# Kernel tuning notes

Hardware: AMD Instinct MI355X
Metric: run time of the kernel (lower is better)

The kernel has to match this reference:

```python
import jax, jax.numpy as jnp
import numpy as np

HEAD_NUM = 16


def setup_inputs() -> dict:
    key = jax.random.key(0)
    k1, k2, k3, k4 = jax.random.split(key, 4)
    B, S, E = 8, 1024, 1024
    inputs = jax.random.normal(k1, (B, S, E), dtype=jnp.float32)
    W_Query = jax.random.normal(k2, (E, E), dtype=jnp.float32) * 0.05
    W_Key = jax.random.normal(k3, (E, E), dtype=jnp.float32) * 0.05
    W_Value = jax.random.normal(k4, (E, E), dtype=jnp.float32) * 0.05
    return {"inputs": inputs, "W_Query": W_Query, "W_Key": W_Key, "W_Value": W_Value}


def reference(inputs, W_Query, W_Key, W_Value):
    B, S, E = inputs.shape
    H = HEAD_NUM
    D = E // H
    # QKV projections: [B,S,E] @ [E,E] -> [B,S,E]
    q = jnp.einsum('bse,ef->bsf', inputs, W_Query).reshape(B, S, H, D)
    k = jnp.einsum('bse,ef->bsf', inputs, W_Key).reshape(B, S, H, D)
    v = jnp.einsum('bse,ef->bsf', inputs, W_Value).reshape(B, S, H, D)
    # NOTE: original has NO 1/sqrt(D) scaling.
    scores = jnp.einsum('bihd,bjhd->bhij', q, k)  # [B,H,S,S]
    att = jax.nn.softmax(scores, axis=-1)
    out = jnp.einsum('bhij,bjhd->bihd', att, v).reshape(B, S, E)
    return jax.nn.relu(out)
```

## Files before the change

kernel.cpp:

```cpp
#include <hip/hip_runtime.h>
#include <cstdint>
#include <cstddef>

#define B_ 8
#define S_ 1024
#define E_ 1024
#define H_ 16
#define D_ 64
#define M_ (B_*S_)

typedef _Float16 f16;
typedef __attribute__((ext_vector_type(8))) _Float16 f16x8;
typedef __attribute__((ext_vector_type(4))) _Float16 f16x4;
typedef __attribute__((ext_vector_type(4))) float  f32x4;
typedef __attribute__((ext_vector_type(16))) float f32x16;
typedef __attribute__((ext_vector_type(4))) int    int4v;
typedef __attribute__((ext_vector_type(2))) int    int2v;

__device__ __forceinline__ f32x4 mfma16(f16x8 a, f16x8 b, f32x4 c) {
  return __builtin_amdgcn_mfma_f32_16x16x32_f16(a, b, c, 0, 0, 0);
}
__device__ __forceinline__ f32x16 mfma32(f16x8 a, f16x8 b, f32x16 c) {
  return __builtin_amdgcn_mfma_f32_32x32x16_f16(a, b, c, 0, 0, 0);
}
__device__ __forceinline__ void gll16(const f16* g, f16* l) {
  __builtin_amdgcn_global_load_lds(
      (const __attribute__((address_space(1))) void*)g,
      (__attribute__((address_space(3))) void*)l, 16, 0, 0);
}
__device__ __forceinline__ int pkrtz(float lo, float hi) {
  return __builtin_bit_cast(int, __builtin_amdgcn_cvt_pkrtz(lo, hi));
}

__global__ __launch_bounds__(256) void presplit_kernel(
    const float* __restrict__ X, f16* __restrict__ Xf) {
  size_t i = ((size_t)blockIdx.x * 256 + threadIdx.x) * 8;
  f32x4 v0 = *(const f32x4*)&X[i];
  f32x4 v1 = *(const f32x4*)&X[i + 4];
  f16x8 hv;
#pragma unroll
  for (int j = 0; j < 4; ++j) {
    hv[j] = (f16)v0[j];
    hv[j + 4] = (f16)v1[j];
  }
  *(f16x8*)&Xf[i] = hv;
}

__global__ __launch_bounds__(512) void wt_conv3_kernel(
    const float* __restrict__ Wq, const float* __restrict__ Wk,
    const float* __restrict__ Wv, f16* __restrict__ oq, f16* __restrict__ ok,
    f16* __restrict__ ov) {
  const float* W = blockIdx.z == 0 ? Wq : (blockIdx.z == 1 ? Wk : Wv);
  f16* o = blockIdx.z == 0 ? oq : (blockIdx.z == 1 ? ok : ov);
  const float scl = blockIdx.z == 0 ? 1.4426950408889634f : 1.0f;
  __shared__ float t[64][65];
  const int f0 = blockIdx.x * 64, e0 = blockIdx.y * 64;
  const int tx = threadIdx.x, ty = threadIdx.y;
#pragma unroll
  for (int j = 0; j < 8; ++j)
    t[ty + 8 * j][tx] = W[(size_t)(e0 + ty + 8 * j) * E_ + f0 + tx];
  __syncthreads();
#pragma unroll
  for (int j = 0; j < 8; ++j)
    o[(size_t)(f0 + ty + 8 * j) * E_ + e0 + tx] =
        (f16)(t[tx][ty + 8 * j] * scl);
}

__global__ __launch_bounds__(256) void gemm_qkv_kernel(
    const f16* __restrict__ Xf,
    const f16* __restrict__ Wq, const f16* __restrict__ Wk,
    const f16* __restrict__ Wv,
    f16* __restrict__ Qh, f16* __restrict__ Ql,
    f16* __restrict__ Kh, f16* __restrict__ Kl, f16* __restrict__ Vt) {
  __shared__ f16 sA[128][64], sB[128][64];
  const int bid = blockIdx.x;
  const int xcd = bid & 7, idx = bid >> 3;
  const int mb = xcd * 8 + idx / 24;
  const int nb = idx % 24;
  const int z = nb >> 3;
  const int n0 = (nb & 7) * 128, m0 = mb * 128;
  const f16* __restrict__ Bt = z == 0 ? Wq : (z == 1 ? Wk : Wv);
  const int tid = threadIdx.x;
  const int lane = tid & 63, w = tid >> 6;
  const int wm = (w >> 1) * 64, wn = (w & 1) * 64;
  const int fr = lane & 15, fg = lane >> 4;
  f32x4 acc[4][4] = {};
  for (int k0 = 0; k0 < E_; k0 += 64) {
#pragma unroll
    for (int i = 0; i < 4; ++i) {
      int ci = tid + i * 256;
      int r = ci >> 3, cl = ci & 7;
      int cs = (cl ^ (r & 7)) * 8;
      gll16(Xf + (size_t)(m0 + r) * E_ + k0 + cs, &sA[0][0] + ci * 8);
      gll16(Bt + (size_t)(n0 + r) * E_ + k0 + cs, &sB[0][0] + ci * 8);
    }
    __syncthreads();
#pragma unroll
    for (int kh2 = 0; kh2 < 2; ++kh2) {
      f16x8 ah[4];
#pragma unroll
      for (int mi = 0; mi < 4; ++mi) {
        int rA = wm + mi * 16 + fr;
        ah[mi] = *(const f16x8*)&sA[rA][(((kh2 * 4 + fg) ^ (rA & 7))) * 8];
      }
#pragma unroll
      for (int ni = 0; ni < 4; ++ni) {
        int rB = wn + ni * 16 + fr;
        f16x8 bh = *(const f16x8*)&sB[rB][(((kh2 * 4 + fg) ^ (rB & 7))) * 8];
#pragma unroll
        for (int mi = 0; mi < 4; ++mi)
          acc[mi][ni] = mfma16(ah[mi], bh, acc[mi][ni]);
      }
    }
    __syncthreads();
  }
  if (z < 2) {
    f16* Oh = z == 0 ? Qh : Kh;
    f16* Ol = z == 0 ? Ql : Kl;
#pragma unroll
    for (int mi = 0; mi < 4; ++mi)
#pragma unroll
      for (int ni = 0; ni < 4; ++ni)
#pragma unroll
        for (int r = 0; r < 4; ++r) {
          int row = m0 + wm + mi * 16 + (lane >> 4) * 4 + r;
          int col = n0 + wn + ni * 16 + fr;
          float v = acc[mi][ni][r];
          int bb = row >> 10, s = row & 1023;
          int hd = col >> 6, d = col & 63;
          size_t idx2 = ((size_t)(bb * H_ + hd) * S_ + s) * D_ + d;
          f16 hh = (f16)v;
          Oh[idx2] = hh;
          Ol[idx2] = (f16)(v - (float)hh);
        }
  } else {
#pragma unroll
    for (int mi = 0; mi < 4; ++mi)
#pragma unroll
      for (int ni = 0; ni < 4; ++ni) {
        int row = m0 + wm + mi * 16 + (lane >> 4) * 4;
        int col = n0 + wn + ni * 16 + fr;
        int bb = row >> 10, s = row & 1023;
        int hd = col >> 6, d = col & 63;
        f16x4 p;
#pragma unroll
        for (int r = 0; r < 4; ++r) p[r] = (f16)acc[mi][ni][r];
        *(f16x4*)&Vt[((size_t)(bb * H_ + hd) * D_ + d) * S_ + s] = p;
      }
  }
}

__global__ __launch_bounds__(256, 2) void attn_kernel(
    const f16* __restrict__ Qh, const f16* __restrict__ Ql,
    const f16* __restrict__ Kh, const f16* __restrict__ Kl,
    const f16* __restrict__ Vt, float* __restrict__ out) {
  __shared__ f16 sKh[2][64][64], sKl[2][64][64], sV[2][64][64];
  const int bid = blockIdx.x;
  const int idx = bid >> 3;
  const int bh = (bid & 7) * 16 + (idx >> 2);
  const int qb = idx & 3;
  const int hd = bh & 15, bb = bh >> 4;
  const int tid = threadIdx.x;
  const int lane = tid & 63, w = tid >> 6;
  const int cq = lane & 31, h = lane >> 5;
  const size_t base = (size_t)bh * (S_ * D_);
  const f16* Qh_p = Qh + base;
  const f16* Ql_p = Ql + base;
  const f16* Kh_p = Kh + base;
  const f16* Kl_p = Kl + base;
  const f16* Vt_p = Vt + base;
  const int q0 = qb * 256 + w * 64;

  f16x8 qh_[2][4], ql_[2][4];
#pragma unroll
  for (int qf = 0; qf < 2; ++qf)
#pragma unroll
    for (int ks = 0; ks < 4; ++ks) {
      size_t off = (size_t)(q0 + qf * 32 + cq) * D_ + ks * 16 + 8 * h;
      qh_[qf][ks] = *(const f16x8*)&Qh_p[off];
      ql_[qf][ks] = *(const f16x8*)&Ql_p[off];
    }

  float m_run[2] = {-1e30f, -1e30f};
  float l_run[2] = {0.f, 0.f};
  f32x16 O[2][2] = {};

#define STAGE(buf, kb)                                                        \
  {                                                                           \
    _Pragma("unroll")                                                         \
    for (int half = 0; half < 2; ++half) {                                    \
      int ci = tid + half * 256;                                              \
      int row = ci >> 3, cl = ci & 7;                                         \
      int cs = cl ^ (row & 7);                                                \
      gll16(Kh_p + (size_t)((kb) + row) * D_ + cs * 8, &sKh[buf][0][0] + ci * 8); \
      gll16(Kl_p + (size_t)((kb) + row) * D_ + cs * 8, &sKl[buf][0][0] + ci * 8); \
      gll16(Vt_p + (size_t)row * S_ + (kb) + cs * 8, &sV[buf][0][0] + ci * 8);    \
    }                                                                         \
  }

  STAGE(0, 0);
  int cur = 0;
  for (int t = 0; t < 16; ++t) {
    __builtin_amdgcn_s_barrier();
    if (t < 15) {
      STAGE(cur ^ 1, (t + 1) * 64);
      asm volatile("s_waitcnt vmcnt(6)" ::: "memory");
    } else {
      asm volatile("s_waitcnt vmcnt(0)" ::: "memory");
    }
    __builtin_amdgcn_sched_barrier(0);
    __builtin_amdgcn_s_barrier();

    f32x16 sc[2][2] = {};
    __builtin_amdgcn_s_setprio(1);
#pragma unroll
    for (int f = 0; f < 2; ++f)
#pragma unroll
      for (int ks = 0; ks < 4; ++ks) {
        int row = f * 32 + cq;
        int cc = ((2 * ks + h) ^ (cq & 7)) * 8;
        f16x8 kh = *(const f16x8*)&sKh[cur][row][cc];
        f16x8 kl = *(const f16x8*)&sKl[cur][row][cc];
#pragma unroll
        for (int qf = 0; qf < 2; ++qf) {
          sc[qf][f] = mfma32(kh, qh_[qf][ks], sc[qf][f]);
          sc[qf][f] = mfma32(kl, qh_[qf][ks], sc[qf][f]);
          sc[qf][f] = mfma32(kh, ql_[qf][ks], sc[qf][f]);
        }
      }
    __builtin_amdgcn_s_setprio(0);

#pragma unroll
    for (int qf = 0; qf < 2; ++qf) {
      float t8[8];
#pragma unroll
      for (int i = 0; i < 8; ++i)
        t8[i] = fmaxf(fmaxf(sc[qf][0][i], sc[qf][0][i + 8]),
                      fmaxf(sc[qf][1][i], sc[qf][1][i + 8]));
      float pmax = fmaxf(fmaxf(fmaxf(t8[0], t8[4]), fmaxf(t8[1], t8[5])),
                         fmaxf(fmaxf(t8[2], t8[6]), fmaxf(t8[3], t8[7])));
      pmax = fmaxf(pmax, __shfl_xor(pmax, 32));
      if (__any(pmax > m_run[qf] + 11.0f)) {
        float mn = fmaxf(m_run[qf], pmax);
        float scale = __builtin_amdgcn_exp2f(m_run[qf] - mn);
        m_run[qf] = mn;
        l_run[qf] *= scale;
#pragma unroll
        for (int df = 0; df < 2; ++df)
#pragma unroll
          for (int i = 0; i < 16; ++i) O[qf][df][i] *= scale;
      }
      float rs0 = 0.f, rs1 = 0.f, rs2 = 0.f, rs3 = 0.f;
#pragma unroll
      for (int f = 0; f < 2; ++f)
#pragma unroll
        for (int r = 0; r < 16; ++r) {
          float p = __builtin_amdgcn_exp2f(sc[qf][f][r] - m_run[qf]);
          if ((r & 3) == 0) rs0 += p;
          else if ((r & 3) == 1) rs1 += p;
          else if ((r & 3) == 2) rs2 += p;
          else rs3 += p;
          sc[qf][f][r] = p;
        }
      float rs = (rs0 + rs1) + (rs2 + rs3);
      rs += __shfl_xor(rs, 32);
      l_run[qf] += rs;

      f16x8 pf[4];
#pragma unroll
      for (int f = 0; f < 2; ++f)
#pragma unroll
        for (int ksl = 0; ksl < 2; ++ksl) {
          int b0 = 8 * ksl;
          int a1 = pkrtz(sc[qf][f][b0 + 0], sc[qf][f][b0 + 1]);
          int b1 = pkrtz(sc[qf][f][b0 + 4], sc[qf][f][b0 + 5]);
          int2v r1 = __builtin_amdgcn_permlane32_swap(a1, b1, false, false);
          int a2 = pkrtz(sc[qf][f][b0 + 2], sc[qf][f][b0 + 3]);
          int b2 = pkrtz(sc[qf][f][b0 + 6], sc[qf][f][b0 + 7]);
          int2v r2 = __builtin_amdgcn_permlane32_swap(a2, b2, false, false);
          int4v wd;
          wd[0] = r1[0]; wd[1] = r2[0]; wd[2] = r1[1]; wd[3] = r2[1];
          pf[2 * f + ksl] = __builtin_bit_cast(f16x8, wd);
        }

      __builtin_amdgcn_s_setprio(1);
#pragma unroll
      for (int ks = 0; ks < 4; ++ks) {
        int cc = ((2 * ks + h) ^ (cq & 7)) * 8;
#pragma unroll
        for (int df = 0; df < 2; ++df) {
          f16x8 vf = *(const f16x8*)&sV[cur][df * 32 + cq][cc];
          O[qf][df] = mfma32(vf, pf[ks], O[qf][df]);
        }
      }
      __builtin_amdgcn_s_setprio(0);
    }
    cur ^= 1;
  }

#pragma unroll
  for (int qf = 0; qf < 2; ++qf) {
    float inv = 1.0f / l_run[qf];
    int s = q0 + qf * 32 + cq;
    float* orow = out + ((size_t)bb * S_ + s) * E_ + hd * 64;
#pragma unroll
    for (int df = 0; df < 2; ++df)
#pragma unroll
      for (int g = 0; g < 4; ++g) {
        f32x4 vv;
#pragma unroll
        for (int j = 0; j < 4; ++j)
          vv[j] = fmaxf(O[qf][df][4 * g + j] * inv, 0.f);
        *(f32x4*)&orow[df * 32 + 8 * g + 4 * h] = vv;
      }
  }
}

extern "C" void kernel_launch(void* const* d_in, const int* in_sizes, int n_in,
                              void* d_out, int out_size, void* d_ws, size_t ws_size,
                              hipStream_t stream) {
  const float* X  = (const float*)d_in[0];
  const float* Wq = (const float*)d_in[1];
  const float* Wk = (const float*)d_in[2];
  const float* Wv = (const float*)d_in[3];
  float* out = (float*)d_out;
  char* ws = (char*)d_ws;

  const size_t WSZ = (size_t)E_ * E_ * sizeof(f16);
  const size_t QSZ = (size_t)M_ * E_ * sizeof(f16);
  f16* Wqf = (f16*)(ws);
  f16* Wkf = (f16*)(ws + WSZ);
  f16* Wvf = (f16*)(ws + 2 * WSZ);
  char* p = ws + 3 * WSZ;
  f16* Xf = (f16*)(p);
  f16* Qh = (f16*)(p + QSZ);
  f16* Ql = (f16*)(p + 2 * QSZ);
  f16* Kh = (f16*)(p + 3 * QSZ);
  f16* Kl = (f16*)(p + 4 * QSZ);
  f16* Vt = (f16*)(p + 5 * QSZ);

  presplit_kernel<<<4096, 256, 0, stream>>>(X, Xf);
  wt_conv3_kernel<<<dim3(16, 16, 3), dim3(64, 8), 0, stream>>>(
      Wq, Wk, Wv, Wqf, Wkf, Wvf);

  gemm_qkv_kernel<<<1536, 256, 0, stream>>>(
      Xf, Wqf, Wkf, Wvf, Qh, Ql, Kh, Kl, Vt);

  attn_kernel<<<512, 256, 0, stream>>>(Qh, Ql, Kh, Kl, Vt, out);
}
```

Measured before the change: 160.6 us.

## Permute K/V layout for split 64-bit LDS reads, fixed-offset softmax, shared V fragments

The K and transposed V producers now write with a row-dependent swap of 4-element halves, and the attention kernel reads LDS fragments as two 64-bit loads whose order depends on the lane, aimed at cutting LDS bank conflicts. The online softmax drops the per-block max reduction before exponentiation. It starts from a fixed offset of 64, exponentiates first, and rescales only when the exponentiated values exceed a threshold, using a log to update the running offset. The PV loop is hoisted out of the per-qf loop so each V fragment read feeds both query fragments. This halves V LDS reads but keeps more registers live, and the fixed offset risks overflow or underflow if scores fall outside the assumed range.

```diff
diff --git a/kernel.cpp b/kernel.cpp
--- a/kernel.cpp
+++ b/kernel.cpp
@@ -16,6 +16,7 @@
 typedef __attribute__((ext_vector_type(16))) float f32x16;
 typedef __attribute__((ext_vector_type(4))) int    int4v;
 typedef __attribute__((ext_vector_type(2))) int    int2v;
+typedef __attribute__((ext_vector_type(2))) unsigned long long u64x2;
 
 __device__ __forceinline__ f32x4 mfma16(f16x8 a, f16x8 b, f32x4 c) {
   return __builtin_amdgcn_mfma_f32_16x16x32_f16(a, b, c, 0, 0, 0);
@@ -30,6 +31,13 @@
 }
 __device__ __forceinline__ int pkrtz(float lo, float hi) {
   return __builtin_bit_cast(int, __builtin_amdgcn_cvt_pkrtz(lo, hi));
+}
+__device__ __forceinline__ f16x8 rdpair(const f16* rowp, int L, int rsw, int sel8) {
+  const char* p = (const char*)rowp + (((L ^ rsw) << 4));
+  u64x2 t;
+  t[0] = *(const unsigned long long*)(p + sel8);
+  t[1] = *(const unsigned long long*)(p + (sel8 ^ 8));
+  return __builtin_bit_cast(f16x8, t);
 }
 
 __global__ __launch_bounds__(256) void presplit_kernel(
@@ -128,6 +136,7 @@
           float v = acc[mi][ni][r];
           int bb = row >> 10, s = row & 1023;
           int hd = col >> 6, d = col & 63;
+          if (z == 1 && (s & 8)) d ^= 4;
           size_t idx2 = ((size_t)(bb * H_ + hd) * S_ + s) * D_ + d;
           f16 hh = (f16)v;
           Oh[idx2] = hh;
@@ -142,6 +151,7 @@
         int col = n0 + wn + ni * 16 + fr;
         int bb = row >> 10, s = row & 1023;
         int hd = col >> 6, d = col & 63;
+        if (d & 8) s ^= 4;
         f16x4 p;
 #pragma unroll
         for (int r = 0; r < 4; ++r) p[r] = (f16)acc[mi][ni][r];
@@ -163,6 +173,8 @@
   const int tid = threadIdx.x;
   const int lane = tid & 63, w = tid >> 6;
   const int cq = lane & 31, h = lane >> 5;
+  const int rsw = cq & 7;
+  const int sel8 = cq & 8;
   const size_t base = (size_t)bh * (S_ * D_);
   const f16* Qh_p = Qh + base;
   const f16* Ql_p = Ql + base;
@@ -181,7 +193,7 @@
       ql_[qf][ks] = *(const f16x8*)&Ql_p[off];
     }
 
-  float m_run[2] = {-1e30f, -1e30f};
+  float m_run[2] = {64.f, 64.f};
   float l_run[2] = {0.f, 0.f};
   f32x16 O[2][2] = {};
 
@@ -214,13 +226,13 @@
     f32x16 sc[2][2] = {};
     __builtin_amdgcn_s_setprio(1);
 #pragma unroll
-    for (int f = 0; f < 2; ++f)
+    for (int f = 0; f < 2; ++f) {
+      const f16* rK  = &sKh[cur][f * 32 + cq][0];
+      const f16* rKl = &sKl[cur][f * 32 + cq][0];
 #pragma unroll
       for (int ks = 0; ks < 4; ++ks) {
-        int row = f * 32 + cq;
-        int cc = ((2 * ks + h) ^ (cq & 7)) * 8;
-        f16x8 kh = *(const f16x8*)&sKh[cur][row][cc];
-        f16x8 kl = *(const f16x8*)&sKl[cur][row][cc];
+        f16x8 kh = rdpair(rK,  2 * ks + h, rsw, sel8);
+        f16x8 kl = rdpair(rKl, 2 * ks + h, rsw, sel8);
 #pragma unroll
         for (int qf = 0; qf < 2; ++qf) {
           sc[qf][f] = mfma32(kh, qh_[qf][ks], sc[qf][f]);
@@ -228,45 +240,53 @@
           sc[qf][f] = mfma32(kh, ql_[qf][ks], sc[qf][f]);
         }
       }
+    }
     __builtin_amdgcn_s_setprio(0);
 
+    f16x8 pf[2][4];
 #pragma unroll
     for (int qf = 0; qf < 2; ++qf) {
+#pragma unroll
+      for (int f = 0; f < 2; ++f)
+#pragma unroll
+        for (int r = 0; r < 16; ++r)
+          sc[qf][f][r] = __builtin_amdgcn_exp2f(sc[qf][f][r] - m_run[qf]);
       float t8[8];
 #pragma unroll
       for (int i = 0; i < 8; ++i)
         t8[i] = fmaxf(fmaxf(sc[qf][0][i], sc[qf][0][i + 8]),
                       fmaxf(sc[qf][1][i], sc[qf][1][i + 8]));
-      float pmax = fmaxf(fmaxf(fmaxf(t8[0], t8[4]), fmaxf(t8[1], t8[5])),
-                         fmaxf(fmaxf(t8[2], t8[6]), fmaxf(t8[3], t8[7])));
-      pmax = fmaxf(pmax, __shfl_xor(pmax, 32));
-      if (__any(pmax > m_run[qf] + 11.0f)) {
-        float mn = fmaxf(m_run[qf], pmax);
-        float scale = __builtin_amdgcn_exp2f(m_run[qf] - mn);
-        m_run[qf] = mn;
-        l_run[qf] *= scale;
+      float pm = fmaxf(fmaxf(fmaxf(t8[0], t8[4]), fmaxf(t8[1], t8[5])),
+                       fmaxf(fmaxf(t8[2], t8[6]), fmaxf(t8[3], t8[7])));
+      pm = fmaxf(pm, __shfl_xor(pm, 32));
+      if (__any(pm > 2048.f)) {
+        float scl = pm > 1.0f ? 1.0f / pm : 1.0f;
+        m_run[qf] += pm > 1.0f ? __builtin_amdgcn_logf(pm) : 0.f;
+        l_run[qf] *= scl;
+#pragma unroll
+        for (int f = 0; f < 2; ++f)
+#pragma unroll
+          for (int r = 0; r < 16; ++r) sc[qf][f][r] *= scl;
 #pragma unroll
         for (int df = 0; df < 2; ++df)
 #pragma unroll
-          for (int i = 0; i < 16; ++i) O[qf][df][i] *= scale;
+          for (int i = 0; i < 16; ++i) O[qf][df][i] *= scl;
       }
       float rs0 = 0.f, rs1 = 0.f, rs2 = 0.f, rs3 = 0.f;
 #pragma unroll
       for (int f = 0; f < 2; ++f)
 #pragma unroll
         for (int r = 0; r < 16; ++r) {
-          float p = __builtin_amdgcn_exp2f(sc[qf][f][r] - m_run[qf]);
+          float p = sc[qf][f][r];
           if ((r & 3) == 0) rs0 += p;
           else if ((r & 3) == 1) rs1 += p;
           else if ((r & 3) == 2) rs2 += p;
           else rs3 += p;
-          sc[qf][f][r] = p;
         }
       float rs = (rs0 + rs1) + (rs2 + rs3);
       rs += __shfl_xor(rs, 32);
       l_run[qf] += rs;
 
-      f16x8 pf[4];
 #pragma unroll
       for (int f = 0; f < 2; ++f)
 #pragma unroll
@@ -280,21 +300,21 @@
           int2v r2 = __builtin_amdgcn_permlane32_swap(a2, b2, false, false);
           int4v wd;
           wd[0] = r1[0]; wd[1] = r2[0]; wd[2] = r1[1]; wd[3] = r2[1];
-          pf[2 * f + ksl] = __builtin_bit_cast(f16x8, wd);
+          pf[qf][2 * f + ksl] = __builtin_bit_cast(f16x8, wd);
         }
-
-      __builtin_amdgcn_s_setprio(1);
-#pragma unroll
-      for (int ks = 0; ks < 4; ++ks) {
-        int cc = ((2 * ks + h) ^ (cq & 7)) * 8;
-#pragma unroll
-        for (int df = 0; df < 2; ++df) {
-          f16x8 vf = *(const f16x8*)&sV[cur][df * 32 + cq][cc];
-          O[qf][df] = mfma32(vf, pf[ks], O[qf][df]);
-        }
-      }
-      __builtin_amdgcn_s_setprio(0);
-    }
+    }
+
+    __builtin_amdgcn_s_setprio(1);
+#pragma unroll
+    for (int ks = 0; ks < 4; ++ks) {
+#pragma unroll
+      for (int df = 0; df < 2; ++df) {
+        f16x8 vf = rdpair(&sV[cur][df * 32 + cq][0], 2 * ks + h, rsw, sel8);
+        O[0][df] = mfma32(vf, pf[0][ks], O[0][df]);
+        O[1][df] = mfma32(vf, pf[1][ks], O[1][df]);
+      }
+    }
+    __builtin_amdgcn_s_setprio(0);
     cur ^= 1;
   }
 
```

Result: slower. 192.5 us (+19.8%).
